# Kernel optimization log

Measured on AMD Instinct MI355X. Metric: run time of the kernel, lower is better.

The kernel has to match this reference:

```python
import jax, jax.numpy as jnp
import numpy as np

B, C, H, W = 4, 256, 64, 64
E = C // 8  # embedding_channels = inChannels // k


def setup_inputs() -> dict:
    key = jax.random.key(0)
    ks = jax.random.split(key, 9)
    sc = 1.0 / np.sqrt(C)
    so = 1.0 / np.sqrt(E)
    return {
        "x": jax.random.normal(ks[0], (B, C, H, W), dtype=jnp.float32),
        "Wk": jax.random.normal(ks[1], (E, C), dtype=jnp.float32) * sc,
        "bk": jax.random.normal(ks[2], (E,), dtype=jnp.float32) * 0.01,
        "Wq": jax.random.normal(ks[3], (E, C), dtype=jnp.float32) * sc,
        "bq": jax.random.normal(ks[4], (E,), dtype=jnp.float32) * 0.01,
        "Wv": jax.random.normal(ks[5], (E, C), dtype=jnp.float32) * sc,
        "bv": jax.random.normal(ks[6], (E,), dtype=jnp.float32) * 0.01,
        "Wo": jax.random.normal(ks[7], (C, E), dtype=jnp.float32) * so,
        "bo": jax.random.normal(ks[8], (C,), dtype=jnp.float32) * 0.01,
    }


def reference(x, Wk, bk, Wq, bq, Wv, bv, Wo, bo):
    b, c, h, w = x.shape
    n = h * w
    gamma = jnp.float32(0.5)  # non-learned branch (learned=False default)

    def conv1x1(inp, Wt, bt):
        # 1x1 conv == channel-mixing matmul: [b,c,h,w] x [e,c] -> [b,e,h,w]
        return jnp.einsum('bchw,ec->behw', inp, Wt) + bt[None, :, None, None]

    f = conv1x1(x, Wk, bk).reshape(b, -1, n)  # key   [b,E,N]
    g = conv1x1(x, Wq, bq).reshape(b, -1, n)  # query [b,E,N]
    hx = conv1x1(x, Wv, bv).reshape(b, -1, n)  # value [b,E,N]

    s = jnp.einsum('bei,bej->bij', f, g)       # f^T @ g, [b,N,N]
    beta = jax.nn.softmax(s, axis=1)           # softmax over dim 1 (rows) as in torch
    v = jnp.einsum('bei,bij->bej', hx, beta)   # h @ beta, [b,E,N]
    v = v.reshape(b, -1, h, w)

    o = jnp.einsum('behw,ce->bchw', v, Wo) + bo[None, :, None, None]
    y = gamma * o + x
    return y, o, gamma
```

## Files before the change

kernel.cpp:

```cpp
#include <hip/hip_runtime.h>

#define B_ 4
#define C_ 256
#define N_ 4096
#define E_ 32

typedef _Float16 f16x8 __attribute__((ext_vector_type(8)));
typedef _Float16 f16x4 __attribute__((ext_vector_type(4)));
typedef float f32x4 __attribute__((ext_vector_type(4)));

#define LOG2E 1.44269504088896f

__global__ __launch_bounds__(256) void proj_kernel(
    const float* __restrict__ x,
    const float* __restrict__ Wk, const float* __restrict__ bk,
    const float* __restrict__ Wq, const float* __restrict__ bq,
    const float* __restrict__ Wv, const float* __restrict__ bv,
    const float* __restrict__ Wo,
    _Float16* __restrict__ Qb, _Float16* __restrict__ Kb, _Float16* __restrict__ Vb,
    _Float16* __restrict__ Wof16, float* __restrict__ out)
{
    const int m = blockIdx.x >> 8;
    if (m == 3) {
        for (int i4 = threadIdx.x; i4 < (C_ * E_) / 4; i4 += 256) {
            float4 wv = ((const float4*)Wo)[i4];
            f16x4 tp = {(_Float16)wv.x, (_Float16)wv.y, (_Float16)wv.z, (_Float16)wv.w};
            *(f16x4*)&Wof16[i4 * 4] = tp;
        }
        if (threadIdx.x == 0)
            out[(size_t)2 * B_ * C_ * N_] = 0.5f;
        return;
    }
    const int rem = blockIdx.x & 255;
    const int b   = rem >> 6;
    const int n0  = (rem & 63) << 6;
    const int t    = threadIdx.x;
    const int lane = t & 63;
    const int wave = t >> 6;
    const int l15  = lane & 15;
    const int quad = lane >> 4;

    __shared__ _Float16 xT[64][264];
    __shared__ _Float16 Wl[32][264];

    const float* W    = (m == 0) ? Wk : (m == 1) ? Wq : Wv;
    const float* bias = (m == 0) ? bk : (m == 1) ? bq : bv;

    for (int i4 = t; i4 < (E_ * C_) / 4; i4 += 256) {
        float4 wv = ((const float4*)W)[i4];
        int e = (i4 * 4) >> 8, c = (i4 * 4) & 255;
        f16x4 tp = {(_Float16)wv.x, (_Float16)wv.y, (_Float16)wv.z, (_Float16)wv.w};
        *(f16x4*)&Wl[e][c] = tp;
    }
    for (int i4 = t; i4 < (64 * 256) / 4; i4 += 256) {
        int j4 = (i4 & 15) * 4;
        int c  = i4 >> 4;
        float4 xv = *(const float4*)(x + (size_t)(b * C_ + c) * N_ + n0 + j4);
        xT[j4 + 0][c] = (_Float16)xv.x;
        xT[j4 + 1][c] = (_Float16)xv.y;
        xT[j4 + 2][c] = (_Float16)xv.z;
        xT[j4 + 3][c] = (_Float16)xv.w;
    }
    __syncthreads();

    f16x8 Bf[8];
    for (int kk = 0; kk < 8; ++kk)
        Bf[kk] = *(const f16x8*)&xT[wave * 16 + l15][kk * 32 + quad * 8];

    const float sc = (m == 1) ? LOG2E : 1.0f;
    for (int et = 0; et < 2; ++et) {
        f32x4 acc = {0.f, 0.f, 0.f, 0.f};
        for (int kk = 0; kk < 8; ++kk) {
            f16x8 Af = *(const f16x8*)&Wl[et * 16 + l15][kk * 32 + quad * 8];
            acc = __builtin_amdgcn_mfma_f32_16x16x32_f16(Af, Bf[kk], acc, 0, 0, 0);
        }
        const int n = n0 + wave * 16 + l15;
        for (int r = 0; r < 4; ++r) {
            const int e = et * 16 + quad * 4 + r;
            float v = (acc[r] + bias[e]) * sc;
            _Float16 hv = (_Float16)v;
            if      (m == 0) Kb[(size_t)(b * N_ + n) * E_ + e] = hv;
            else if (m == 1) Qb[(size_t)(b * N_ + n) * E_ + e] = hv;
            else             Vb[(size_t)(b * E_ + e) * N_ + n] = hv;
        }
    }
}

__global__ __launch_bounds__(512, 4) void attn_kernel(
    const _Float16* __restrict__ Qb, const _Float16* __restrict__ Kb,
    const _Float16* __restrict__ Vb, const _Float16* __restrict__ Wof16,
    const float* __restrict__ bo, const float* __restrict__ x,
    float* __restrict__ out)
{
    const int wave = threadIdx.x >> 6;
    const int lane = threadIdx.x & 63;
    const int l15  = lane & 15, quad = lane >> 4;
    const int jg   = blockIdx.x;
    const int b    = jg >> 8;
    const int j0   = (jg & 255) << 4;

    __shared__ __align__(16) char pbuf[8][4224];
    __shared__ float    mls[8][2][16];
    __shared__ _Float16 Om[16][36];

    _Float16 (*pb)[132] = (_Float16 (*)[132])(pbuf[wave]);

    f16x8 Qf = *(const f16x8*)(Qb + (size_t)(b * N_ + j0 + l15) * E_ + quad * 8);

    f32x4 O0 = {0, 0, 0, 0}, O1 = {0, 0, 0, 0};
    float mrow = -1e30f, lsum = 0.f;

    const _Float16* Kbase = Kb + (size_t)b * N_ * E_;
    const _Float16* Vbase = Vb + (size_t)b * E_ * N_;
    const int ibase = wave << 9;

    f16x8 Kf[8];
    for (int s = 0; s < 8; ++s)
        Kf[s] = *(const f16x8*)(Kbase + (size_t)(ibase + s * 16 + l15) * E_ + quad * 8);

    for (int it = 0; it < 4; ++it) {
        const int i0 = ibase + it * 128;
        f32x4 S[8];
        for (int s = 0; s < 8; ++s) {
            f32x4 z = {0, 0, 0, 0};
            S[s] = __builtin_amdgcn_mfma_f32_16x16x32_f16(Kf[s], Qf, z, 0, 0, 0);
        }
        float t0, t1, t2, t3;
        t0 = fmaxf(fmaxf(S[0][0], S[0][1]), fmaxf(S[0][2], S[0][3]));
        t1 = fmaxf(fmaxf(S[1][0], S[1][1]), fmaxf(S[1][2], S[1][3]));
        t2 = fmaxf(fmaxf(S[2][0], S[2][1]), fmaxf(S[2][2], S[2][3]));
        t3 = fmaxf(fmaxf(S[3][0], S[3][1]), fmaxf(S[3][2], S[3][3]));
        float mA = fmaxf(fmaxf(t0, t1), fmaxf(t2, t3));
        t0 = fmaxf(fmaxf(S[4][0], S[4][1]), fmaxf(S[4][2], S[4][3]));
        t1 = fmaxf(fmaxf(S[5][0], S[5][1]), fmaxf(S[5][2], S[5][3]));
        t2 = fmaxf(fmaxf(S[6][0], S[6][1]), fmaxf(S[6][2], S[6][3]));
        t3 = fmaxf(fmaxf(S[7][0], S[7][1]), fmaxf(S[7][2], S[7][3]));
        float mx = fmaxf(mA, fmaxf(fmaxf(t0, t1), fmaxf(t2, t3)));
        mx = fmaxf(mx, __shfl_xor(mx, 16));
        mx = fmaxf(mx, __shfl_xor(mx, 32));
        float mnew  = fmaxf(mrow, mx);
        float alpha = exp2f(mrow - mnew);
        mrow = mnew;
        float ss[8];
        for (int s = 0; s < 8; ++s) {
            float p0 = exp2f(S[s][0] - mnew);
            float p1 = exp2f(S[s][1] - mnew);
            float p2 = exp2f(S[s][2] - mnew);
            float p3 = exp2f(S[s][3] - mnew);
            S[s][0] = p0; S[s][1] = p1; S[s][2] = p2; S[s][3] = p3;
            ss[s] = (p0 + p1) + (p2 + p3);
        }
        float ps = ((ss[0] + ss[1]) + (ss[2] + ss[3]))
                 + ((ss[4] + ss[5]) + (ss[6] + ss[7]));
        lsum = lsum * alpha + ps;
        for (int r = 0; r < 4; ++r) { O0[r] *= alpha; O1[r] *= alpha; }
        for (int s = 0; s < 8; ++s) {
            f16x4 tp = {(_Float16)S[s][0], (_Float16)S[s][1],
                        (_Float16)S[s][2], (_Float16)S[s][3]};
            *(f16x4*)&pb[l15][s * 16 + quad * 4] = tp;
        }
        f16x8 P[4];
        for (int kc = 0; kc < 4; ++kc)
            P[kc] = *(const f16x8*)&pb[l15][kc * 32 + quad * 8];
        f16x8 Va[4], Vc[4];
        for (int kc = 0; kc < 4; ++kc) {
            Va[kc] = *(const f16x8*)(Vbase + (size_t)l15 * N_ + i0 + kc * 32 + quad * 8);
            Vc[kc] = *(const f16x8*)(Vbase + (size_t)(16 + l15) * N_ + i0 + kc * 32 + quad * 8);
        }
        const int inext = (it < 3) ? (i0 + 128) : ibase;
        for (int s = 0; s < 8; ++s)
            Kf[s] = *(const f16x8*)(Kbase + (size_t)(inext + s * 16 + l15) * E_ + quad * 8);
        for (int kc = 0; kc < 4; ++kc) {
            O0 = __builtin_amdgcn_mfma_f32_16x16x32_f16(Va[kc], P[kc], O0, 0, 0, 0);
            O1 = __builtin_amdgcn_mfma_f32_16x16x32_f16(Vc[kc], P[kc], O1, 0, 0, 0);
        }
    }

    lsum += __shfl_xor(lsum, 16);
    lsum += __shfl_xor(lsum, 32);
    if (quad == 0) { mls[wave][0][l15] = mrow; mls[wave][1][l15] = lsum; }
    __syncthreads();

    float M = -1e30f, ms[8], ls[8];
    for (int s = 0; s < 8; ++s) {
        ms[s] = mls[s][0][l15]; ls[s] = mls[s][1][l15];
        M = fmaxf(M, ms[s]);
    }
    float L = 0.f;
    for (int s = 0; s < 8; ++s) L += ls[s] * exp2f(ms[s] - M);
    const float w = exp2f(mrow - M) / L;

    float (*osum)[34] = (float (*)[34])(pbuf[wave]);
    *(f32x4*)&osum[l15][quad * 4]      = O0 * w;
    *(f32x4*)&osum[l15][16 + quad * 4] = O1 * w;
    __syncthreads();

    {
        const int j = threadIdx.x >> 5;
        const int e = threadIdx.x & 31;
        float a = 0.f;
        for (int s = 0; s < 8; ++s)
            a += ((const float (*)[34])(pbuf[s]))[j][e];
        Om[j][e] = (_Float16)a;
    }
    __syncthreads();

    f16x8 Bf2 = *(const f16x8*)&Om[l15][quad * 8];
    float* out_y = out + (size_t)b * C_ * N_;
    float* out_o = out + (size_t)B_ * C_ * N_ + (size_t)b * C_ * N_;
    const float* xb = x + (size_t)b * C_ * N_;
    for (int ct = 0; ct < 2; ++ct) {
        const int c0 = wave * 32 + ct * 16;
        f16x8 Af = *(const f16x8*)(Wof16 + (size_t)(c0 + l15) * E_ + quad * 8);
        f32x4 z = {0, 0, 0, 0};
        f32x4 acc = __builtin_amdgcn_mfma_f32_16x16x32_f16(Af, Bf2, z, 0, 0, 0);
        for (int r = 0; r < 4; ++r) {
            const int c = c0 + quad * 4 + r;
            size_t idx = (size_t)c * N_ + j0 + l15;
            float ov = acc[r] + bo[c];
            out_o[idx] = ov;
            out_y[idx] = 0.5f * ov + xb[idx];
        }
    }
}

extern "C" void kernel_launch(void* const* d_in, const int* in_sizes, int n_in,
                              void* d_out, int out_size, void* d_ws, size_t ws_size,
                              hipStream_t stream)
{
    const float* x  = (const float*)d_in[0];
    const float* Wk = (const float*)d_in[1];
    const float* bk = (const float*)d_in[2];
    const float* Wq = (const float*)d_in[3];
    const float* bq = (const float*)d_in[4];
    const float* Wv = (const float*)d_in[5];
    const float* bv = (const float*)d_in[6];
    const float* Wo = (const float*)d_in[7];
    const float* bo = (const float*)d_in[8];
    float* out = (float*)d_out;

    char* ws = (char*)d_ws;
    _Float16* Qb    = (_Float16*)(ws);
    _Float16* Kb    = (_Float16*)(ws + (1u << 20));
    _Float16* Vb    = (_Float16*)(ws + (2u << 20));
    _Float16* Wof16 = (_Float16*)(ws + (3u << 20));

    proj_kernel<<<dim3(3 * B_ * (N_ / 64) + 256), dim3(256), 0, stream>>>(
        x, Wk, bk, Wq, bq, Wv, bv, Wo, Qb, Kb, Vb, Wof16, out);
    attn_kernel<<<dim3(B_ * (N_ / 16)), dim3(512), 0, stream>>>(
        Qb, Kb, Vb, Wof16, bo, x, out);
}
```

Before: 149.4 us.

## Shrink attention inner tile to 32 keys to raise occupancy

Reduces the per-iteration key tile in the attention loop from 128 to 32 keys (16 iterations instead of 4) and drops the software-prefetched K register array, cutting register use and per-wave LDS buffer size. The launch-bounds minimum blocks hint is raised from 4 to 6 so more waves can be resident and hide latency. The trade-off is more online-softmax rescaling steps, more shuffles and LDS round-trips per key, and no explicit prefetch of the next K tile.

```diff
diff --git a/kernel.cpp b/kernel.cpp
--- a/kernel.cpp
+++ b/kernel.cpp
@@ -86,7 +86,7 @@
     }
 }
 
-__global__ __launch_bounds__(512, 4) void attn_kernel(
+__global__ __launch_bounds__(512, 6) void attn_kernel(
     const _Float16* __restrict__ Qb, const _Float16* __restrict__ Kb,
     const _Float16* __restrict__ Vb, const _Float16* __restrict__ Wof16,
     const float* __restrict__ bo, const float* __restrict__ x,
@@ -99,81 +99,51 @@
     const int b    = jg >> 8;
     const int j0   = (jg & 255) << 4;
 
-    __shared__ __align__(16) char pbuf[8][4224];
+    __shared__ __align__(16) char pbuf[8][2176];
     __shared__ float    mls[8][2][16];
-    __shared__ _Float16 Om[16][36];
-
-    _Float16 (*pb)[132] = (_Float16 (*)[132])(pbuf[wave]);
+    __shared__ _Float16 Om[16][40];
+
+    _Float16 (*pb)[40] = (_Float16 (*)[40])(pbuf[wave]);
 
     f16x8 Qf = *(const f16x8*)(Qb + (size_t)(b * N_ + j0 + l15) * E_ + quad * 8);
 
     f32x4 O0 = {0, 0, 0, 0}, O1 = {0, 0, 0, 0};
     float mrow = -1e30f, lsum = 0.f;
 
-    const _Float16* Kbase = Kb + (size_t)b * N_ * E_;
-    const _Float16* Vbase = Vb + (size_t)b * E_ * N_;
-    const int ibase = wave << 9;
-
-    f16x8 Kf[8];
-    for (int s = 0; s < 8; ++s)
-        Kf[s] = *(const f16x8*)(Kbase + (size_t)(ibase + s * 16 + l15) * E_ + quad * 8);
-
-    for (int it = 0; it < 4; ++it) {
-        const int i0 = ibase + it * 128;
-        f32x4 S[8];
-        for (int s = 0; s < 8; ++s) {
-            f32x4 z = {0, 0, 0, 0};
-            S[s] = __builtin_amdgcn_mfma_f32_16x16x32_f16(Kf[s], Qf, z, 0, 0, 0);
-        }
-        float t0, t1, t2, t3;
-        t0 = fmaxf(fmaxf(S[0][0], S[0][1]), fmaxf(S[0][2], S[0][3]));
-        t1 = fmaxf(fmaxf(S[1][0], S[1][1]), fmaxf(S[1][2], S[1][3]));
-        t2 = fmaxf(fmaxf(S[2][0], S[2][1]), fmaxf(S[2][2], S[2][3]));
-        t3 = fmaxf(fmaxf(S[3][0], S[3][1]), fmaxf(S[3][2], S[3][3]));
-        float mA = fmaxf(fmaxf(t0, t1), fmaxf(t2, t3));
-        t0 = fmaxf(fmaxf(S[4][0], S[4][1]), fmaxf(S[4][2], S[4][3]));
-        t1 = fmaxf(fmaxf(S[5][0], S[5][1]), fmaxf(S[5][2], S[5][3]));
-        t2 = fmaxf(fmaxf(S[6][0], S[6][1]), fmaxf(S[6][2], S[6][3]));
-        t3 = fmaxf(fmaxf(S[7][0], S[7][1]), fmaxf(S[7][2], S[7][3]));
-        float mx = fmaxf(mA, fmaxf(fmaxf(t0, t1), fmaxf(t2, t3)));
+    const _Float16* Kp  = Kb + (size_t)b * N_ * E_ + (size_t)(wave << 9) * E_;
+    const _Float16* Vp  = Vb + (size_t)b * E_ * N_ + (wave << 9);
+
+    for (int it = 0; it < 16; ++it) {
+        const int i0 = it * 32;
+        f16x8 K0 = *(const f16x8*)(Kp + (size_t)(i0 + l15) * E_ + quad * 8);
+        f16x8 K1 = *(const f16x8*)(Kp + (size_t)(i0 + 16 + l15) * E_ + quad * 8);
+        f16x8 Va = *(const f16x8*)(Vp + (size_t)l15 * N_ + i0 + quad * 8);
+        f16x8 Vc = *(const f16x8*)(Vp + (size_t)(16 + l15) * N_ + i0 + quad * 8);
+        f32x4 z = {0, 0, 0, 0};
+        f32x4 S0 = __builtin_amdgcn_mfma_f32_16x16x32_f16(K0, Qf, z, 0, 0, 0);
+        f32x4 S1 = __builtin_amdgcn_mfma_f32_16x16x32_f16(K1, Qf, z, 0, 0, 0);
+        float a0 = fmaxf(S0[0], S0[1]), a1 = fmaxf(S0[2], S0[3]);
+        float a2 = fmaxf(S1[0], S1[1]), a3 = fmaxf(S1[2], S1[3]);
+        float mx = fmaxf(fmaxf(a0, a1), fmaxf(a2, a3));
         mx = fmaxf(mx, __shfl_xor(mx, 16));
         mx = fmaxf(mx, __shfl_xor(mx, 32));
         float mnew  = fmaxf(mrow, mx);
         float alpha = exp2f(mrow - mnew);
         mrow = mnew;
-        float ss[8];
-        for (int s = 0; s < 8; ++s) {
-            float p0 = exp2f(S[s][0] - mnew);
-            float p1 = exp2f(S[s][1] - mnew);
-            float p2 = exp2f(S[s][2] - mnew);
-            float p3 = exp2f(S[s][3] - mnew);
-            S[s][0] = p0; S[s][1] = p1; S[s][2] = p2; S[s][3] = p3;
-            ss[s] = (p0 + p1) + (p2 + p3);
-        }
-        float ps = ((ss[0] + ss[1]) + (ss[2] + ss[3]))
-                 + ((ss[4] + ss[5]) + (ss[6] + ss[7]));
+        float p00 = exp2f(S0[0] - mnew), p01 = exp2f(S0[1] - mnew);
+        float p02 = exp2f(S0[2] - mnew), p03 = exp2f(S0[3] - mnew);
+        float p10 = exp2f(S1[0] - mnew), p11 = exp2f(S1[1] - mnew);
+        float p12 = exp2f(S1[2] - mnew), p13 = exp2f(S1[3] - mnew);
+        float ps = ((p00 + p01) + (p02 + p03)) + ((p10 + p11) + (p12 + p13));
         lsum = lsum * alpha + ps;
         for (int r = 0; r < 4; ++r) { O0[r] *= alpha; O1[r] *= alpha; }
-        for (int s = 0; s < 8; ++s) {
-            f16x4 tp = {(_Float16)S[s][0], (_Float16)S[s][1],
-                        (_Float16)S[s][2], (_Float16)S[s][3]};
-            *(f16x4*)&pb[l15][s * 16 + quad * 4] = tp;
-        }
-        f16x8 P[4];
-        for (int kc = 0; kc < 4; ++kc)
-            P[kc] = *(const f16x8*)&pb[l15][kc * 32 + quad * 8];
-        f16x8 Va[4], Vc[4];
-        for (int kc = 0; kc < 4; ++kc) {
-            Va[kc] = *(const f16x8*)(Vbase + (size_t)l15 * N_ + i0 + kc * 32 + quad * 8);
-            Vc[kc] = *(const f16x8*)(Vbase + (size_t)(16 + l15) * N_ + i0 + kc * 32 + quad * 8);
-        }
-        const int inext = (it < 3) ? (i0 + 128) : ibase;
-        for (int s = 0; s < 8; ++s)
-            Kf[s] = *(const f16x8*)(Kbase + (size_t)(inext + s * 16 + l15) * E_ + quad * 8);
-        for (int kc = 0; kc < 4; ++kc) {
-            O0 = __builtin_amdgcn_mfma_f32_16x16x32_f16(Va[kc], P[kc], O0, 0, 0, 0);
-            O1 = __builtin_amdgcn_mfma_f32_16x16x32_f16(Vc[kc], P[kc], O1, 0, 0, 0);
-        }
+        f16x4 w0 = {(_Float16)p00, (_Float16)p01, (_Float16)p02, (_Float16)p03};
+        f16x4 w1 = {(_Float16)p10, (_Float16)p11, (_Float16)p12, (_Float16)p13};
+        *(f16x4*)&pb[l15][quad * 4]      = w0;
+        *(f16x4*)&pb[l15][16 + quad * 4] = w1;
+        f16x8 P = *(const f16x8*)&pb[l15][quad * 8];
+        O0 = __builtin_amdgcn_mfma_f32_16x16x32_f16(Va, P, O0, 0, 0, 0);
+        O1 = __builtin_amdgcn_mfma_f32_16x16x32_f16(Vc, P, O1, 0, 0, 0);
     }
 
     lsum += __shfl_xor(lsum, 16);
```

New measurement: 148.7 us. No clear change (-0.5%).
